# Kernel optimization log

Hardware: AMD Instinct MI355X
Metric: run time of the kernel (lower is better)

## Reference

```python
import jax, jax.numpy as jnp
import numpy as np

B, F, K, VOCAB = 16384, 39, 64, 1000000
HID = [10, 5, 3]


def setup_inputs() -> dict:
    key = jax.random.key(0)
    ks = jax.random.split(key, 12)
    feature = jax.random.randint(ks[0], (B, F), 0, VOCAB)
    v_table = jax.random.normal(ks[1], (VOCAB, K), dtype=jnp.float32) * 0.01
    w_table = jax.random.normal(ks[2], (VOCAB, 1), dtype=jnp.float32) * 0.01
    w0 = jnp.zeros((1,), dtype=jnp.float32)
    d_in = F * K
    def lin(kw, kb, din, dout):
        s = 1.0 / np.sqrt(din)
        W = jax.random.uniform(kw, (din, dout), minval=-s, maxval=s, dtype=jnp.float32)
        b = jax.random.uniform(kb, (dout,), minval=-s, maxval=s, dtype=jnp.float32)
        return W, b
    W0, b0 = lin(ks[3], ks[4], d_in, HID[0])
    W1, b1 = lin(ks[5], ks[6], HID[0], HID[1])
    W2, b2 = lin(ks[7], ks[8], HID[1], HID[2])
    W3, b3 = lin(ks[9], ks[10], HID[2], 1)
    return {"feature": feature, "v_table": v_table, "w_table": w_table, "w0": w0,
            "W0": W0, "b0": b0, "W1": W1, "b1": b1, "W2": W2, "b2": b2, "W3": W3, "b3": b3}


def reference(feature, v_table, w_table, w0, W0, b0, W1, b1, W2, b2, W3, b3):
    # Embedding gather: [B, F, K]
    V = v_table[feature]
    # FM pairwise term sum_{i<j} V_i . V_j = 0.5*(||sum_i V_i||^2 - sum_i ||V_i||^2)
    s = jnp.sum(V, axis=1)                       # [B, K]
    fm = 0.5 * (jnp.sum(s * s, axis=-1) - jnp.sum(V * V, axis=(1, 2)))  # [B]
    # Linear (first-order) term
    lin = jnp.sum(w_table[feature], axis=(1, 2))  # [B]
    # Tiny DNN on flattened embeddings
    h = V.reshape(V.shape[0], -1)                 # [B, F*K]
    h = jax.nn.relu(h @ W0 + b0)
    h = jax.nn.relu(h @ W1 + b1)
    h = jax.nn.relu(h @ W2 + b2)
    dnn = h @ W3 + b3                             # [B, 1]
    return fm[:, None] + lin[:, None] + w0 + dnn  # [B, 1]
```

## Files before the change

kernel.cpp:

```cpp
#include <hip/hip_runtime.h>
#include <hip/hip_bf16.h>

#define NF 39
#define NK 64
#define NROW (NF * NK)

__device__ __forceinline__ float bf_lo(unsigned u) { return __uint_as_float(u << 16); }
__device__ __forceinline__ float bf_hi(unsigned u) { return __uint_as_float(u & 0xffff0000u); }

__device__ __forceinline__ unsigned f2bf(float f) {
    unsigned u = __float_as_uint(f);
    return (u + 0x7fffu + ((u >> 16) & 1u)) >> 16;
}

__global__ __launch_bounds__(512, 2)
void deepfm_kernel(const int* __restrict__ feature,
                   const float* __restrict__ v_table,
                   const float* __restrict__ w_table,
                   const float* __restrict__ w0s,
                   const float* __restrict__ W0,
                   const float* __restrict__ b0,
                   const float* __restrict__ W1,
                   const float* __restrict__ b1,
                   const float* __restrict__ W2,
                   const float* __restrict__ b2,
                   const float* __restrict__ W3,
                   const float* __restrict__ b3,
                   float* __restrict__ out)
{
    __shared__ unsigned w0_lds[5 * NROW];

    for (int i = threadIdx.x; i < NROW; i += 512) {
        #pragma unroll
        for (int jp = 0; jp < 5; ++jp) {
            unsigned lo = f2bf(W0[i * 10 + 2 * jp]);
            unsigned hi = f2bf(W0[i * 10 + 2 * jp + 1]);
            w0_lds[jp * NROW + i] = lo | (hi << 16);
        }
    }
    __syncthreads();

    const int lane = threadIdx.x & 63;
    const int wave = threadIdx.x >> 6;
    const int s0   = blockIdx.x * 32 + wave * 4;
    const int sg   = lane >> 4;
    const int kq   = lane & 15;

    const int* fptr = feature + (size_t)(s0 + sg) * NF;

    float h0p[4][10];
    float sv[4], sq[4];
    float lin = 0.f;
    #pragma unroll
    for (int i = 0; i < 4; ++i) {
        sv[i] = 0.f; sq[i] = 0.f;
        #pragma unroll
        for (int j = 0; j < 10; ++j) h0p[i][j] = 0.f;
    }

    #pragma unroll 2
    for (int f = 0; f < NF; ++f) {
        const int idx = fptr[f];
        lin += w_table[idx];
        const float4 v4 = ((const float4*)(v_table + ((size_t)(unsigned)idx << 6)))[kq];
        const float vv[4] = { v4.x, v4.y, v4.z, v4.w };
        #pragma unroll
        for (int i = 0; i < 4; ++i) {
            sv[i] += vv[i];
            sq[i]  = fmaf(vv[i], vv[i], sq[i]);
        }
        #pragma unroll
        for (int jp = 0; jp < 5; ++jp) {
            const uint4 u = *(const uint4*)&w0_lds[jp * NROW + f * NK + kq * 4];
            h0p[0][2*jp]   = fmaf(vv[0], bf_lo(u.x), h0p[0][2*jp]);
            h0p[0][2*jp+1] = fmaf(vv[0], bf_hi(u.x), h0p[0][2*jp+1]);
            h0p[1][2*jp]   = fmaf(vv[1], bf_lo(u.y), h0p[1][2*jp]);
            h0p[1][2*jp+1] = fmaf(vv[1], bf_hi(u.y), h0p[1][2*jp+1]);
            h0p[2][2*jp]   = fmaf(vv[2], bf_lo(u.z), h0p[2][2*jp]);
            h0p[2][2*jp+1] = fmaf(vv[2], bf_hi(u.z), h0p[2][2*jp+1]);
            h0p[3][2*jp]   = fmaf(vv[3], bf_lo(u.w), h0p[3][2*jp]);
            h0p[3][2*jp+1] = fmaf(vv[3], bf_hi(u.w), h0p[3][2*jp+1]);
        }
    }

    float t = 0.f;
    #pragma unroll
    for (int i = 0; i < 4; ++i) t += fmaf(sv[i], sv[i], -sq[i]);
    float hj[10];
    #pragma unroll
    for (int j = 0; j < 10; ++j)
        hj[j] = (h0p[0][j] + h0p[1][j]) + (h0p[2][j] + h0p[3][j]);
    #pragma unroll
    for (int m = 1; m < 16; m <<= 1) {
        t += __shfl_xor(t, m, 64);
        #pragma unroll
        for (int j = 0; j < 10; ++j)
            hj[j] += __shfl_xor(hj[j], m, 64);
    }

    const float w0v = w0s[0];
    float h0v[10];
    #pragma unroll
    for (int j = 0; j < 10; ++j) h0v[j] = fmaxf(hj[j] + b0[j], 0.f);
    float h1[5];
    #pragma unroll
    for (int p = 0; p < 5; ++p) {
        float a = b1[p];
        #pragma unroll
        for (int j = 0; j < 10; ++j) a = fmaf(h0v[j], W1[j * 5 + p], a);
        h1[p] = fmaxf(a, 0.f);
    }
    float h2[3];
    #pragma unroll
    for (int q = 0; q < 3; ++q) {
        float a = b2[q];
        #pragma unroll
        for (int p = 0; p < 5; ++p) a = fmaf(h1[p], W2[p * 3 + q], a);
        h2[q] = fmaxf(a, 0.f);
    }
    float dnn = b3[0];
    #pragma unroll
    for (int q = 0; q < 3; ++q) dnn = fmaf(h2[q], W3[q], dnn);

    if (kq == 0) out[s0 + sg] = 0.5f * t + lin + w0v + dnn;
}

extern "C" void kernel_launch(void* const* d_in, const int* in_sizes, int n_in,
                              void* d_out, int out_size, void* d_ws, size_t ws_size,
                              hipStream_t stream) {
    const int*   feature = (const int*)  d_in[0];
    const float* v_table = (const float*)d_in[1];
    const float* w_table = (const float*)d_in[2];
    const float* w0s     = (const float*)d_in[3];
    const float* W0      = (const float*)d_in[4];
    const float* b0      = (const float*)d_in[5];
    const float* W1      = (const float*)d_in[6];
    const float* b1      = (const float*)d_in[7];
    const float* W2      = (const float*)d_in[8];
    const float* b2      = (const float*)d_in[9];
    const float* W3      = (const float*)d_in[10];
    const float* b3      = (const float*)d_in[11];

    deepfm_kernel<<<dim3(512), dim3(512), 0, stream>>>(
        feature, v_table, w_table, w0s, W0, b0, W1, b1, W2, b2, W3, b3,
        (float*)d_out);
}
```

Baseline: 44.46 us.

## Use fp16 packed dot-products with k-pair LDS layout for first DNN layer

Stores W0 in LDS as fp16, packed in pairs along the embedding dimension and laid out per output neuron, in place of bf16 pairs packed across outputs. The inner loop converts gathered embedding values to packed fp16 and accumulates with v_dot2_f32_f16, so there are 10 accumulators instead of 40. The aim is to halve the VALU FMA count and cut register pressure. In exchange the activations lose precision through round-toward-zero fp16 conversion, and each thread issues more, smaller LDS loads (10 uint2 instead of 5 uint4).

```diff
diff --git a/kernel.cpp b/kernel.cpp
--- a/kernel.cpp
+++ b/kernel.cpp
@@ -3,14 +3,13 @@
 
 #define NF 39
 #define NK 64
-#define NROW (NF * NK)
+#define NRP (NF * NK / 2)
 
-__device__ __forceinline__ float bf_lo(unsigned u) { return __uint_as_float(u << 16); }
-__device__ __forceinline__ float bf_hi(unsigned u) { return __uint_as_float(u & 0xffff0000u); }
+typedef _Float16 f16x2 __attribute__((ext_vector_type(2)));
+typedef __fp16  h16x2 __attribute__((ext_vector_type(2)));
 
-__device__ __forceinline__ unsigned f2bf(float f) {
-    unsigned u = __float_as_uint(f);
-    return (u + 0x7fffu + ((u >> 16) & 1u)) >> 16;
+__device__ __forceinline__ unsigned short f16bits(float f) {
+    return __builtin_bit_cast(unsigned short, (_Float16)f);
 }
 
 __global__ __launch_bounds__(512, 2)
@@ -28,15 +27,14 @@
                    const float* __restrict__ b3,
                    float* __restrict__ out)
 {
-    __shared__ unsigned w0_lds[5 * NROW];
+    __shared__ unsigned w0_lds[10 * NRP];
 
-    for (int i = threadIdx.x; i < NROW; i += 512) {
-        #pragma unroll
-        for (int jp = 0; jp < 5; ++jp) {
-            unsigned lo = f2bf(W0[i * 10 + 2 * jp]);
-            unsigned hi = f2bf(W0[i * 10 + 2 * jp + 1]);
-            w0_lds[jp * NROW + i] = lo | (hi << 16);
-        }
+    for (int i = threadIdx.x; i < 10 * NRP; i += 512) {
+        const int j  = i / NRP;
+        const int rp = i - j * NRP;
+        unsigned lo = f16bits(W0[(2 * rp)     * 10 + j]);
+        unsigned hi = f16bits(W0[(2 * rp + 1) * 10 + j]);
+        w0_lds[j * NRP + rp] = lo | (hi << 16);
     }
     __syncthreads();
 
@@ -48,60 +46,64 @@
 
     const int* fptr = feature + (size_t)(s0 + sg) * NF;
 
-    float h0p[4][10];
+    float h0[10];
     float sv[4], sq[4];
     float lin = 0.f;
     #pragma unroll
-    for (int i = 0; i < 4; ++i) {
-        sv[i] = 0.f; sq[i] = 0.f;
-        #pragma unroll
-        for (int j = 0; j < 10; ++j) h0p[i][j] = 0.f;
-    }
+    for (int j = 0; j < 10; ++j) h0[j] = 0.f;
+    #pragma unroll
+    for (int i = 0; i < 4; ++i) { sv[i] = 0.f; sq[i] = 0.f; }
 
-    #pragma unroll 2
+    #pragma unroll 3
     for (int f = 0; f < NF; ++f) {
         const int idx = fptr[f];
         lin += w_table[idx];
         const float4 v4 = ((const float4*)(v_table + ((size_t)(unsigned)idx << 6)))[kq];
-        const float vv[4] = { v4.x, v4.y, v4.z, v4.w };
+        sv[0] += v4.x;  sq[0] = fmaf(v4.x, v4.x, sq[0]);
+        sv[1] += v4.y;  sq[1] = fmaf(v4.y, v4.y, sq[1]);
+        sv[2] += v4.z;  sq[2] = fmaf(v4.z, v4.z, sq[2]);
+        sv[3] += v4.w;  sq[3] = fmaf(v4.w, v4.w, sq[3]);
+
+#if __has_builtin(__builtin_amdgcn_fdot2) && __has_builtin(__builtin_amdgcn_cvt_pkrtz)
+        const f16x2 hv01 = __builtin_bit_cast(f16x2, __builtin_amdgcn_cvt_pkrtz(v4.x, v4.y));
+        const f16x2 hv23 = __builtin_bit_cast(f16x2, __builtin_amdgcn_cvt_pkrtz(v4.z, v4.w));
+        const unsigned base = f * 32 + 2 * kq;
         #pragma unroll
-        for (int i = 0; i < 4; ++i) {
-            sv[i] += vv[i];
-            sq[i]  = fmaf(vv[i], vv[i], sq[i]);
+        for (int j = 0; j < 10; ++j) {
+            const uint2 u = *(const uint2*)&w0_lds[j * NRP + base];
+            h0[j] = __builtin_amdgcn_fdot2(hv01, __builtin_bit_cast(f16x2, u.x), h0[j], false);
+            h0[j] = __builtin_amdgcn_fdot2(hv23, __builtin_bit_cast(f16x2, u.y), h0[j], false);
         }
+#else
+        const unsigned base = f * 32 + 2 * kq;
         #pragma unroll
-        for (int jp = 0; jp < 5; ++jp) {
-            const uint4 u = *(const uint4*)&w0_lds[jp * NROW + f * NK + kq * 4];
-            h0p[0][2*jp]   = fmaf(vv[0], bf_lo(u.x), h0p[0][2*jp]);
-            h0p[0][2*jp+1] = fmaf(vv[0], bf_hi(u.x), h0p[0][2*jp+1]);
-            h0p[1][2*jp]   = fmaf(vv[1], bf_lo(u.y), h0p[1][2*jp]);
-            h0p[1][2*jp+1] = fmaf(vv[1], bf_hi(u.y), h0p[1][2*jp+1]);
-            h0p[2][2*jp]   = fmaf(vv[2], bf_lo(u.z), h0p[2][2*jp]);
-            h0p[2][2*jp+1] = fmaf(vv[2], bf_hi(u.z), h0p[2][2*jp+1]);
-            h0p[3][2*jp]   = fmaf(vv[3], bf_lo(u.w), h0p[3][2*jp]);
-            h0p[3][2*jp+1] = fmaf(vv[3], bf_hi(u.w), h0p[3][2*jp+1]);
+        for (int j = 0; j < 10; ++j) {
+            const uint2 u = *(const uint2*)&w0_lds[j * NRP + base];
+            const f16x2 a = __builtin_bit_cast(f16x2, u.x);
+            const f16x2 b = __builtin_bit_cast(f16x2, u.y);
+            h0[j] = fmaf(v4.x, (float)a.x, h0[j]);
+            h0[j] = fmaf(v4.y, (float)a.y, h0[j]);
+            h0[j] = fmaf(v4.z, (float)b.x, h0[j]);
+            h0[j] = fmaf(v4.w, (float)b.y, h0[j]);
         }
+#endif
     }
 
     float t = 0.f;
     #pragma unroll
     for (int i = 0; i < 4; ++i) t += fmaf(sv[i], sv[i], -sq[i]);
-    float hj[10];
-    #pragma unroll
-    for (int j = 0; j < 10; ++j)
-        hj[j] = (h0p[0][j] + h0p[1][j]) + (h0p[2][j] + h0p[3][j]);
     #pragma unroll
     for (int m = 1; m < 16; m <<= 1) {
         t += __shfl_xor(t, m, 64);
         #pragma unroll
         for (int j = 0; j < 10; ++j)
-            hj[j] += __shfl_xor(hj[j], m, 64);
+            h0[j] += __shfl_xor(h0[j], m, 64);
     }
 
     const float w0v = w0s[0];
     float h0v[10];
     #pragma unroll
-    for (int j = 0; j < 10; ++j) h0v[j] = fmaxf(hj[j] + b0[j], 0.f);
+    for (int j = 0; j < 10; ++j) h0v[j] = fmaxf(h0[j] + b0[j], 0.f);
     float h1[5];
     #pragma unroll
     for (int p = 0; p < 5; ++p) {
```

New measurement: 51.91 us. +16.8%, slower.
